# Kernel optimization log

Measured on AMD Instinct MI355X. Metric: run time of the kernel, lower is better.

Reference implementation:

```python
import jax, jax.numpy as jnp
import numpy as np
from jax import lax

# Module config (matches init_kwargs)
C_IN, C_OUT, D_STATE = 512, 256, 16
D_INNER = 2 * C_OUT          # canonical Mamba expand=2
DT_RANK = C_OUT // 16        # ceil(256/16) = 16
D_CONV = 4
BN_EPS = 1e-5


def setup_inputs() -> dict:
    key = jax.random.key(0)
    ks = jax.random.split(key, 16)
    s = 0.02
    B, H, W = 8, 64, 64
    inp = {
        "x": jax.random.normal(ks[0], (B, C_IN, H, W), jnp.float32),
        # lateral 1x1 conv
        "lateral_w": jax.random.normal(ks[1], (C_OUT, C_IN), jnp.float32) * s,
        "lateral_b": jnp.zeros((C_OUT,), jnp.float32),
        # mamba block params
        "in_proj_w": jax.random.normal(ks[2], (2 * D_INNER, C_OUT), jnp.float32) * s,
        "conv1d_w": jax.random.normal(ks[3], (D_INNER, D_CONV), jnp.float32) * s,
        "conv1d_b": jnp.zeros((D_INNER,), jnp.float32),
        "x_proj_w": jax.random.normal(ks[4], (DT_RANK + 2 * D_STATE, D_INNER), jnp.float32) * s,
        "dt_proj_w": jax.random.normal(ks[5], (D_INNER, DT_RANK), jnp.float32) * s,
        "dt_proj_b": jnp.full((D_INNER,), -4.0, jnp.float32),  # softplus -> small dt
        "A_log": jnp.log(jnp.broadcast_to(jnp.arange(1, D_STATE + 1, dtype=jnp.float32), (D_INNER, D_STATE))),  # S4D-real init
        "D_param": jnp.ones((D_INNER,), jnp.float32),
        "out_proj_w": jax.random.normal(ks[6], (C_OUT, D_INNER), jnp.float32) * s,
        # refine: 3x3 conv + BN (eval) + ReLU
        "refine_w": jax.random.normal(ks[7], (C_OUT, C_OUT, 3, 3), jnp.float32) * s,
        "refine_b": jnp.zeros((C_OUT,), jnp.float32),
        "bn_gamma": jnp.ones((C_OUT,), jnp.float32),
        "bn_beta": jnp.zeros((C_OUT,), jnp.float32),
        "bn_mean": jnp.zeros((C_OUT,), jnp.float32),
        "bn_var": jnp.ones((C_OUT,), jnp.float32),
    }
    return inp


def _silu(v):
    return v * jax.nn.sigmoid(v)


def _mamba(u, in_proj_w, conv1d_w, conv1d_b, x_proj_w, dt_proj_w, dt_proj_b,
           A_log, D_param, out_proj_w):
    """Canonical Mamba block on u: (B, L, D) -> (B, L, D)."""
    B, L, D = u.shape
    xz = jnp.einsum('bld,ed->ble', u, in_proj_w)            # (B,L,2*d_inner)
    xm, z = jnp.split(xz, 2, axis=-1)
    # causal depthwise conv1d over L
    xc = xm.transpose(0, 2, 1)                               # (B,d_inner,L)
    xc = lax.conv_general_dilated(xc, conv1d_w[:, None, :], (1,),
                                  [(D_CONV - 1, 0)],
                                  feature_group_count=D_INNER)
    xc = _silu(xc + conv1d_b[None, :, None]).transpose(0, 2, 1)  # (B,L,d_inner)
    proj = jnp.einsum('bld,ed->ble', xc, x_proj_w)           # (B,L,dt_rank+2*N)
    dt_r = proj[..., :DT_RANK]
    B_ssm = proj[..., DT_RANK:DT_RANK + D_STATE]             # (B,L,N)
    C_ssm = proj[..., DT_RANK + D_STATE:]                    # (B,L,N)
    dt = jax.nn.softplus(jnp.einsum('blr,dr->bld', dt_r, dt_proj_w) + dt_proj_b)
    A = -jnp.exp(A_log)                                      # (d_inner,N)

    def step(h, inputs):
        dt_t, B_t, C_t, x_t = inputs                         # (B,d), (B,N), (B,N), (B,d)
        dA = jnp.exp(dt_t[..., None] * A)                    # (B,d,N)
        h = dA * h + dt_t[..., None] * B_t[:, None, :] * x_t[..., None]
        y = jnp.einsum('bdn,bn->bd', h, C_t)
        return h, y

    xs = (dt.transpose(1, 0, 2), B_ssm.transpose(1, 0, 2),
          C_ssm.transpose(1, 0, 2), xc.transpose(1, 0, 2))
    h0 = jnp.zeros((B, D_INNER, D_STATE), u.dtype)
    _, ys = lax.scan(step, h0, xs)                           # (L,B,d_inner)
    y = ys.transpose(1, 0, 2) + xc * D_param
    y = y * _silu(z)
    return jnp.einsum('ble,de->bld', y, out_proj_w)          # (B,L,D)


def reference(x, lateral_w, lateral_b, in_proj_w, conv1d_w, conv1d_b, x_proj_w,
              dt_proj_w, dt_proj_b, A_log, D_param, out_proj_w, refine_w,
              refine_b, bn_gamma, bn_beta, bn_mean, bn_var):
    B, _, H, W = x.shape
    # lateral 1x1 conv
    xl = jnp.einsum('oi,bihw->bohw', lateral_w, x) + lateral_b[None, :, None, None]
    # mamba on flattened spatial sequence, residual add
    u = xl.reshape(B, C_OUT, H * W).transpose(0, 2, 1)        # (B,L,C)
    m = _mamba(u, in_proj_w, conv1d_w, conv1d_b, x_proj_w, dt_proj_w,
               dt_proj_b, A_log, D_param, out_proj_w)
    xr = xl + m.transpose(0, 2, 1).reshape(B, C_OUT, H, W)
    # refine: 3x3 conv + BN(eval) + ReLU
    r = lax.conv_general_dilated(xr, refine_w, (1, 1), [(1, 1), (1, 1)])
    r = r + refine_b[None, :, None, None]
    inv = bn_gamma / jnp.sqrt(bn_var + BN_EPS)
    r = (r - bn_mean[None, :, None, None]) * inv[None, :, None, None] + bn_beta[None, :, None, None]
    return jax.nn.relu(r)
```

## Files before the change

### kernel.cpp

```cpp
#include <hip/hip_runtime.h>
#include <math.h>

#define NB   8
#define CIN  512
#define COUT 256
#define DIN  512
#define LHW  4096
#define NCHK 128
#define CHL  32
#define PW   66
#define PPOS (PW*PW)

typedef __attribute__((ext_vector_type(8))) short bf16x8;
typedef __attribute__((ext_vector_type(4))) float f32x4;
typedef __attribute__((ext_vector_type(2))) float f32x2;

__device__ __forceinline__ float siluf(float v)  { return v / (1.f + __expf(-v)); }
__device__ __forceinline__ float splusf(float v) {
  return fmaxf(v, 0.f) + __logf(1.f + __expf(-fabsf(v)));
}

__device__ __forceinline__ unsigned short f2b(float f) {
  union { float f; unsigned u; } v; v.f = f;
  unsigned r = v.u + 0x7fff + ((v.u >> 16) & 1);
  return (unsigned short)(r >> 16);
}
__device__ __forceinline__ float b2f(unsigned int u) {
  union { unsigned u; float f; } v; v.u = (u & 0xffffu) << 16; return v.f;
}

__device__ __forceinline__ f32x2 pk_fma(f32x2 a, f32x2 b, f32x2 c) {
  f32x2 d;
  asm("v_pk_fma_f32 %0, %1, %2, %3" : "=v"(d) : "v"(a), "v"(b), "v"(c));
  return d;
}
__device__ __forceinline__ f32x2 pk_mul(f32x2 a, f32x2 b) {
  f32x2 d;
  asm("v_pk_mul_f32 %0, %1, %2" : "=v"(d) : "v"(a), "v"(b));
  return d;
}

__device__ __forceinline__ void gload16(const unsigned short* g, unsigned short* l) {
  __builtin_amdgcn_global_load_lds(
      (const __attribute__((address_space(1))) unsigned int*)g,
      (__attribute__((address_space(3))) unsigned int*)l, 16, 0, 0);
}

#define WO1 131072
#define WO2 393216
#define WO3 425984
#define WO4 557056
#define WO5 1146880
__global__ __launch_bounds__(256)
void k_wprep(const float* __restrict__ lw, const float* __restrict__ ipw,
             const float* __restrict__ xpw, const float* __restrict__ opw,
             const float* __restrict__ rw, const float* __restrict__ dtpw,
             unsigned short* __restrict__ wb, unsigned short* __restrict__ wfb) {
  const int i = blockIdx.x * 256 + threadIdx.x;
  if (i < WO1)      wb[i] = f2b(lw[i]);
  else if (i < WO2) wb[i] = f2b(ipw[i - WO1]);
  else if (i < WO3) {
    const int j = i - WO2, row = j >> 9, col = j & 511;
    wb[i] = (row < 48) ? f2b(xpw[row * 512 + col]) : (unsigned short)0;
  }
  else if (i < WO4) wb[i] = f2b(opw[i - WO3]);
  else if (i < WO5) {
    const int j = i - WO4, o = j / 2304, kk = j % 2304;
    const int tap = kk >> 8, ch = kk & 255;
    wb[i] = f2b(rw[(o * 256 + ch) * 9 + tap]);
  }
  else {
    const int j = i - WO5, row = j >> 9, e = j & 511;
    float v = 0.f;
    if (row < 512) {
#pragma unroll
      for (int r = 0; r < 16; ++r)
        v = fmaf(dtpw[row * 16 + r], xpw[r * 512 + e], v);
    } else if (row < 560) {
      v = xpw[(row - 512) * 512 + e];
    }
    wfb[j] = f2b(v);
  }
}

__global__ __launch_bounds__(256)
void k_xpose(const float* __restrict__ x, unsigned short* __restrict__ xt) {
  __shared__ unsigned short Ts[64][80];
  const int b  = blockIdx.z;
  const int k0 = blockIdx.y * 64;
  const int l0 = blockIdx.x * 64;
  const int t  = threadIdx.x;
  const int tx = t & 15, ty = t >> 4;
#pragma unroll
  for (int r = 0; r < 4; ++r) {
    const int k = ty + r * 16;
    float4 v = *(const float4*)(x + ((size_t)b * CIN + k0 + k) * LHW + l0 + tx * 4);
    Ts[tx*4+0][k] = f2b(v.x);
    Ts[tx*4+1][k] = f2b(v.y);
    Ts[tx*4+2][k] = f2b(v.z);
    Ts[tx*4+3][k] = f2b(v.w);
  }
  __syncthreads();
  const int lr = t >> 2, kc = (t & 3) * 16;
  unsigned short* dst = xt + ((size_t)b * LHW + l0 + lr) * CIN + k0 + kc;
  *(uint4*)dst       = *(const uint4*)&Ts[lr][kc];
  *(uint4*)(dst + 8) = *(const uint4*)&Ts[lr][kc + 8];
}

template<int RSA, int RSB, int KTOT>
__device__ __forceinline__ void gemm_loop_128(
    const unsigned short* __restrict__ Ab, const unsigned short* __restrict__ Bb,
    unsigned short (&As)[2][4096], unsigned short (&Bs)[2][4096],
    int t, f32x4 acc[4][4]) {
  const int w = t >> 6, lane = t & 63;
  const int wm = w >> 1, wn = w & 1;
  const int arow = t >> 2;
  const int acol = (((t & 3) ^ ((t >> 3) & 3))) * 8;
  const int fr = lane & 15;
  const int g8 = ((lane >> 4) * 8) ^ (((fr >> 1) & 3) * 8);
  for (int k0 = 0; k0 < KTOT; k0 += 64) {
    __syncthreads();
    gload16(Ab + (size_t)arow * RSA + k0 + acol,             &As[0][w * 512]);
    gload16(Ab + (size_t)(64 + arow) * RSA + k0 + acol,      &As[0][2048 + w*512]);
    gload16(Bb + (size_t)arow * RSB + k0 + acol,             &Bs[0][w * 512]);
    gload16(Bb + (size_t)(64 + arow) * RSB + k0 + acol,      &Bs[0][2048 + w*512]);
    gload16(Ab + (size_t)arow * RSA + k0 + 32 + acol,        &As[1][w * 512]);
    gload16(Ab + (size_t)(64 + arow) * RSA + k0 + 32 + acol, &As[1][2048 + w*512]);
    gload16(Bb + (size_t)arow * RSB + k0 + 32 + acol,        &Bs[1][w * 512]);
    gload16(Bb + (size_t)(64 + arow) * RSB + k0 + 32 + acol, &Bs[1][2048 + w*512]);
    __syncthreads();
#pragma unroll
    for (int h = 0; h < 2; ++h) {
      bf16x8 af[4], bf[4];
#pragma unroll
      for (int f = 0; f < 4; ++f) {
        af[f] = *(const bf16x8*)&As[h][(wm*64 + f*16 + fr) * 32 + g8];
        bf[f] = *(const bf16x8*)&Bs[h][(wn*64 + f*16 + fr) * 32 + g8];
      }
#pragma unroll
      for (int i = 0; i < 4; ++i)
#pragma unroll
        for (int j = 0; j < 4; ++j)
          acc[i][j] = __builtin_amdgcn_mfma_f32_16x16x32_bf16(af[i], bf[j], acc[i][j], 0, 0, 0);
    }
  }
}

__global__ __launch_bounds__(256)
void k_lat_mfma(const unsigned short* __restrict__ xt, const unsigned short* __restrict__ lwb,
                const float* __restrict__ lb, unsigned short* __restrict__ ub) {
  __shared__ __align__(16) unsigned short As[2][4096], Bs[2][4096];
  const int t = threadIdx.x, lane = t & 63, w = t >> 6;
  const int wm = w >> 1, wn = w & 1;
  const int b = blockIdx.z, m0 = blockIdx.y * 128, n0 = blockIdx.x * 128;
  f32x4 acc[4][4] = {};
  gemm_loop_128<512, 512, 512>(xt + ((size_t)b * LHW + m0) * 512,
                               lwb + (size_t)n0 * 512, As, Bs, t, acc);
  const int fr = lane & 15, q4 = (lane >> 4) * 4;
#pragma unroll
  for (int i = 0; i < 4; ++i) {
    const int l = m0 + wm*64 + i*16 + q4;
#pragma unroll
    for (int j = 0; j < 4; ++j) {
      const int o = n0 + wn*64 + j*16 + fr;
      const float bias = lb[o];
      unsigned short* dst = ub + ((size_t)b * LHW + l) * COUT + o;
#pragma unroll
      for (int q = 0; q < 4; ++q)
        dst[(size_t)q * COUT] = f2b(acc[i][j][q] + bias);
    }
  }
}

__global__ __launch_bounds__(256)
void k_inproj_mfma(const unsigned short* __restrict__ ub, const unsigned short* __restrict__ ipwb,
                   unsigned short* __restrict__ xm_b, unsigned short* __restrict__ zsb) {
  __shared__ __align__(16) unsigned short As[2][4096], Bs[2][4096];
  const int t = threadIdx.x, lane = t & 63, w = t >> 6;
  const int wm = w >> 1, wn = w & 1;
  const int b = blockIdx.z, m0 = blockIdx.y * 128, n0 = blockIdx.x * 128;
  f32x4 acc[4][4] = {};
  gemm_loop_128<256, 256, 256>(ub + ((size_t)b * LHW + m0) * 256,
                               ipwb + (size_t)n0 * 256, As, Bs, t, acc);
  const int fr = lane & 15, q4 = (lane >> 4) * 4;
  const bool isz = (n0 >= 512);
#pragma unroll
  for (int i = 0; i < 4; ++i) {
    const int l = m0 + wm*64 + i*16 + q4;
#pragma unroll
    for (int j = 0; j < 4; ++j) {
      const int e = n0 + wn*64 + j*16 + fr;
      if (isz) {
        unsigned short* dst = zsb + ((size_t)b * LHW + l) * DIN + (e - 512);
#pragma unroll
        for (int q = 0; q < 4; ++q)
          dst[(size_t)q * DIN] = f2b(siluf(acc[i][j][q]));
      } else {
        unsigned short* dst = xm_b + ((size_t)b * LHW + l) * DIN + e;
#pragma unroll
        for (int q = 0; q < 4; ++q)
          dst[(size_t)q * DIN] = f2b(acc[i][j][q]);
      }
    }
  }
}

__global__ __launch_bounds__(256)
void k_conv1d(const unsigned short* __restrict__ xm_b, const float* __restrict__ cw,
              const float* __restrict__ cb, unsigned short* __restrict__ xc_b) {
  const int tid = blockIdx.x * 256 + threadIdx.x;
  const int e8 = tid & 63;
  const int lg = tid >> 6;
  const int l0 = (lg & 511) * 8;
  const int b  = lg >> 9;
  const int e0 = e8 * 8;
  float bias[8];
  *(float4*)&bias[0] = *(const float4*)(cb + e0);
  *(float4*)&bias[4] = *(const float4*)(cb + e0 + 4);
  float wv[8][4];
#pragma unroll
  for (int q = 0; q < 8; ++q) {
    float4 w4 = *(const float4*)(cw + (e0 + q) * 4);
    wv[q][0] = w4.x; wv[q][1] = w4.y; wv[q][2] = w4.z; wv[q][3] = w4.w;
  }
  const unsigned short* base = xm_b + ((size_t)b * LHW + l0) * DIN + e0;
  uint4 rows[11];
  const uint4 z4 = make_uint4(0u, 0u, 0u, 0u);
#pragma unroll
  for (int r = 0; r < 11; ++r) {
    const int ll = r - 3;
    rows[r] = (l0 + ll >= 0) ? *(const uint4*)(base + (ptrdiff_t)ll * DIN) : z4;
  }
  unsigned short* outb = xc_b + ((size_t)b * LHW + l0) * DIN + e0;
#pragma unroll
  for (int j = 0; j < 8; ++j) {
    float acc[8];
#pragma unroll
    for (int q = 0; q < 8; ++q) acc[q] = bias[q];
#pragma unroll
    for (int k = 0; k < 4; ++k) {
      const uint4 raw = rows[j + k];
      acc[0] = fmaf(b2f(raw.x),       wv[0][k], acc[0]);
      acc[1] = fmaf(b2f(raw.x >> 16), wv[1][k], acc[1]);
      acc[2] = fmaf(b2f(raw.y),       wv[2][k], acc[2]);
      acc[3] = fmaf(b2f(raw.y >> 16), wv[3][k], acc[3]);
      acc[4] = fmaf(b2f(raw.z),       wv[4][k], acc[4]);
      acc[5] = fmaf(b2f(raw.z >> 16), wv[5][k], acc[5]);
      acc[6] = fmaf(b2f(raw.w),       wv[6][k], acc[6]);
      acc[7] = fmaf(b2f(raw.w >> 16), wv[7][k], acc[7]);
    }
    uint4 o;
    o.x = (unsigned)f2b(siluf(acc[0])) | ((unsigned)f2b(siluf(acc[1])) << 16);
    o.y = (unsigned)f2b(siluf(acc[2])) | ((unsigned)f2b(siluf(acc[3])) << 16);
    o.z = (unsigned)f2b(siluf(acc[4])) | ((unsigned)f2b(siluf(acc[5])) << 16);
    o.w = (unsigned)f2b(siluf(acc[6])) | ((unsigned)f2b(siluf(acc[7])) << 16);
    *(uint4*)(outb + (size_t)j * DIN) = o;
  }
}

__global__ __launch_bounds__(256)
void k_xdt_mfma(const unsigned short* __restrict__ xc_b, const unsigned short* __restrict__ wfb,
                const float* __restrict__ dtpb,
                unsigned short* __restrict__ dtb, float* __restrict__ proj) {
  __shared__ __align__(16) unsigned short As[2][4096], Bs[2][4096];
  const int t = threadIdx.x, lane = t & 63, w = t >> 6;
  const int wm = w >> 1, wn = w & 1;
  const int b = blockIdx.z, m0 = blockIdx.x * 128, n0 = blockIdx.y * 128;
  f32x4 acc[4][4] = {};
  gemm_loop_128<512, 512, 512>(xc_b + ((size_t)b * LHW + m0) * 512,
                               wfb + (size_t)n0 * 512, As, Bs, t, acc);
  const int fr = lane & 15, q4 = (lane >> 4) * 4;
#pragma unroll
  for (int i = 0; i < 4; ++i) {
    const int l = m0 + wm*64 + i*16 + q4;
#pragma unroll
    for (int j = 0; j < 4; ++j) {
      const int c = n0 + wn*64 + j*16 + fr;
      if (c < 512) {
        const float bias = dtpb[c];
        unsigned short* dst = dtb + ((size_t)b * LHW + l) * 512 + c;
#pragma unroll
        for (int q = 0; q < 4; ++q)
          dst[(size_t)q * 512] = f2b(splusf(acc[i][j][q] + bias));
      } else if (c < 560) {
        float* dst = proj + ((size_t)b * LHW + l) * 48 + (c - 512);
#pragma unroll
        for (int q = 0; q < 4; ++q)
          dst[(size_t)q * 48] = acc[i][j][q];
      }
    }
  }
}

__global__ __launch_bounds__(512, 4)
void k_scanA(const float* __restrict__ proj, const unsigned short* __restrict__ dtb,
             const unsigned short* __restrict__ xc_b, const float* __restrict__ A_log,
             float* __restrict__ Sst, float* __restrict__ SDT) {
  __shared__ float prs[CHL * 16];
  const int bx = blockIdx.x;
  const int b = bx >> 7, c = bx & 127;
  const int d = threadIdx.x;
  const size_t rbase = (size_t)b * LHW + c * CHL;
  for (int i = d; i < CHL * 4; i += 512) {
    const int row = i >> 2, c4 = i & 3;
    *(float4*)&prs[row * 16 + c4 * 4] = *(const float4*)(proj + (rbase + row) * 48 + 16 + c4 * 4);
  }
  float An[16];
#pragma unroll
  for (int q = 0; q < 4; ++q) {
    float4 a4 = *(const float4*)(A_log + d*16 + q*4);
    An[q*4+0] = -__expf(a4.x); An[q*4+1] = -__expf(a4.y);
    An[q*4+2] = -__expf(a4.z); An[q*4+3] = -__expf(a4.w);
  }
  f32x2 h2[8];
#pragma unroll
  for (int k = 0; k < 8; ++k) h2[k] = (f32x2){0.f, 0.f};
  const float An0 = An[0];
  bool lin = true;
#pragma unroll
  for (int n = 1; n < 16; ++n)
    lin = lin && (fabsf(An[n] - (n + 1) * An0) <= 1e-4f * fabsf(An[n]));
  float sdt = 0.f;
  const unsigned short* dt0 = dtb + rbase * 512 + d;
  const unsigned short* xc0 = xc_b + rbase * DIN + d;
  __syncthreads();
  for (int i = 0; i < CHL; ++i) {
    const float dt = b2f(dt0[(size_t)i * 512]);
    sdt += dt;
    const float dtx = dt * b2f(xc0[(size_t)i * DIN]);
    const f32x2 dtx2 = (f32x2){dtx, dtx};
    f32x2 dA2[8];
    if (lin) {
      const float e1 = __expf(dt * An0);
      const float e2 = e1*e1, e3 = e2*e1, e4 = e2*e2, e8 = e4*e4;
      const f32x2 e4v = (f32x2){e4, e4}, e8v = (f32x2){e8, e8};
      dA2[0] = (f32x2){e1, e2};
      dA2[1] = (f32x2){e3, e4};
      dA2[2] = pk_mul(dA2[0], e4v);
      dA2[3] = pk_mul(dA2[1], e4v);
      dA2[4] = pk_mul(dA2[0], e8v);
      dA2[5] = pk_mul(dA2[1], e8v);
      dA2[6] = pk_mul(dA2[2], e8v);
      dA2[7] = pk_mul(dA2[3], e8v);
    } else {
#pragma unroll
      for (int k = 0; k < 8; ++k)
        dA2[k] = (f32x2){__expf(dt * An[2*k]), __expf(dt * An[2*k+1])};
    }
    const f32x2* B2 = (const f32x2*)&prs[i * 16];
#pragma unroll
    for (int k = 0; k < 8; ++k)
      h2[k] = pk_fma(dA2[k], h2[k], pk_mul(dtx2, B2[k]));
  }
  float* o = Sst + ((size_t)bx * 512 + d) * 16;
#pragma unroll
  for (int k = 0; k < 4; ++k)
    *(float4*)(o + k*4) = make_float4(h2[2*k].x, h2[2*k].y, h2[2*k+1].x, h2[2*k+1].y);
  SDT[(size_t)bx * 512 + d] = sdt;
}

__global__ __launch_bounds__(256)
void k_scanB(const float* __restrict__ Sst, const float* __restrict__ SDT,
             const float* __restrict__ A_log, float* __restrict__ hst) {
  const int tid = blockIdx.x * 256 + threadIdx.x;
  const int n = tid & 15;
  const int d = (tid >> 4) & 511;
  const int b = tid >> 13;
  const float An = -__expf(A_log[d * 16 + n]);
  float h = 0.f;
  for (int c = 0; c < NCHK; ++c) {
    const size_t idx = (size_t)((b*NCHK + c)*512 + d);
    hst[idx*16 + n] = h;
    h = __expf(SDT[idx] * An) * h + Sst[idx*16 + n];
  }
}

__global__ __launch_bounds__(512, 4)
void k_scanC(const float* __restrict__ proj, const unsigned short* __restrict__ dtb,
             const unsigned short* __restrict__ xc_b,
             const unsigned short* __restrict__ zsb, const float* __restrict__ hst,
             const float* __restrict__ A_log, const float* __restrict__ Dpar,
             unsigned short* __restrict__ ydata) {
  __shared__ float prs[CHL * 32];
  const int bx = blockIdx.x;
  const int b = bx >> 7, c = bx & 127;
  const int d = threadIdx.x;
  const size_t rbase = (size_t)b * LHW + c * CHL;
  for (int i = d; i < CHL * 8; i += 512) {
    const int row = i >> 3, c4 = i & 7;
    *(float4*)&prs[row * 32 + c4 * 4] = *(const float4*)(proj + (rbase + row) * 48 + 16 + c4 * 4);
  }
  float An[16];
#pragma unroll
  for (int q = 0; q < 4; ++q) {
    float4 a4 = *(const float4*)(A_log + d*16 + q*4);
    An[q*4+0] = -__expf(a4.x); An[q*4+1] = -__expf(a4.y);
    An[q*4+2] = -__expf(a4.z); An[q*4+3] = -__expf(a4.w);
  }
  f32x2 h2[8];
  {
    const float* hsrc = hst + ((size_t)bx * 512 + d) * 16;
#pragma unroll
    for (int k = 0; k < 8; ++k)
      h2[k] = *(const f32x2*)(hsrc + 2*k);
  }
  const float An0 = An[0];
  bool lin = true;
#pragma unroll
  for (int n = 1; n < 16; ++n)
    lin = lin && (fabsf(An[n] - (n + 1) * An0) <= 1e-4f * fabsf(An[n]));
  const float dp = Dpar[d];
  const unsigned short* dt0 = dtb + rbase * 512 + d;
  const unsigned short* xc0 = xc_b + rbase * DIN + d;
  const unsigned short* zs0 = zsb + rbase * DIN + d;
  unsigned short* y0 = ydata + rbase * DIN + d;
  __syncthreads();
  for (int i = 0; i < CHL; ++i) {
    const float dt = b2f(dt0[(size_t)i * 512]);
    const float xt = b2f(xc0[(size_t)i * DIN]);
    const float zv = b2f(zs0[(size_t)i * DIN]);
    const float dtx = dt * xt;
    const f32x2 dtx2 = (f32x2){dtx, dtx};
    f32x2 dA2[8];
    if (lin) {
      const float e1 = __expf(dt * An0);
      const float e2 = e1*e1, e3 = e2*e1, e4 = e2*e2, e8 = e4*e4;
      const f32x2 e4v = (f32x2){e4, e4}, e8v = (f32x2){e8, e8};
      dA2[0] = (f32x2){e1, e2};
      dA2[1] = (f32x2){e3, e4};
      dA2[2] = pk_mul(dA2[0], e4v);
      dA2[3] = pk_mul(dA2[1], e4v);
      dA2[4] = pk_mul(dA2[0], e8v);
      dA2[5] = pk_mul(dA2[1], e8v);
      dA2[6] = pk_mul(dA2[2], e8v);
      dA2[7] = pk_mul(dA2[3], e8v);
    } else {
#pragma unroll
      for (int k = 0; k < 8; ++k)
        dA2[k] = (f32x2){__expf(dt * An[2*k]), __expf(dt * An[2*k+1])};
    }
    const f32x2* B2 = (const f32x2*)&prs[i * 32];
    const f32x2* C2 = (const f32x2*)&prs[i * 32 + 16];
    f32x2 ya = (f32x2){0.f, 0.f}, yb = (f32x2){0.f, 0.f};
#pragma unroll
    for (int k = 0; k < 8; ++k) {
      h2[k] = pk_fma(dA2[k], h2[k], pk_mul(dtx2, B2[k]));
      if (k & 1) yb = pk_fma(h2[k], C2[k], yb);
      else       ya = pk_fma(h2[k], C2[k], ya);
    }
    const float y = (ya.x + ya.y) + (yb.x + yb.y);
    const float ov = (y + xt * dp) * zv;
    y0[(size_t)i * DIN] = f2b(ov);
  }
}

__global__ __launch_bounds__(256)
void k_outproj_mfma(const unsigned short* __restrict__ ydata, const unsigned short* __restrict__ opwb,
                    const unsigned short* __restrict__ ub, unsigned short* __restrict__ xrp) {
  __shared__ __align__(16) unsigned short As[2][4096], Bs[2][4096];
  const int t = threadIdx.x, lane = t & 63, w = t >> 6;
  const int wm = w >> 1, wn = w & 1;
  const int b = blockIdx.z, m0 = blockIdx.y * 128, n0 = blockIdx.x * 128;
  f32x4 acc[4][4] = {};
  gemm_loop_128<512, 512, 512>(ydata + ((size_t)b * LHW + m0) * 512,
                               opwb + (size_t)n0 * 512, As, Bs, t, acc);
  const int fr = lane & 15, q4 = (lane >> 4) * 4;
#pragma unroll
  for (int i = 0; i < 4; ++i) {
    const int lbase = m0 + wm*64 + i*16 + q4;
#pragma unroll
    for (int q = 0; q < 4; ++q) {
      const int l = lbase + q;
      const int pos = ((l >> 6) + 1) * PW + (l & 63) + 1;
#pragma unroll
      for (int j = 0; j < 4; ++j) {
        const int o = n0 + wn*64 + j*16 + fr;
        const float r = b2f(ub[((size_t)b * LHW + l) * COUT + o]);
        xrp[((size_t)b * PPOS + pos) * COUT + o] = f2b(acc[i][j][q] + r);
      }
    }
  }
}

__global__ __launch_bounds__(256)
void k_refine_mfma(const unsigned short* __restrict__ Aw,
                   const unsigned short* __restrict__ xrp,
                   const float* __restrict__ rb, const float* __restrict__ bng,
                   const float* __restrict__ bnb, const float* __restrict__ bnm,
                   const float* __restrict__ bnv, float* __restrict__ out) {
  __shared__ __align__(16) unsigned short As[4][4096], Bs[4][4096];
  const int t = threadIdx.x;
  const int lane = t & 63;
  const int w = t >> 6;
  const int wm = w >> 1, wn = w & 1;
  const int b  = blockIdx.z;
  const int m0 = blockIdx.y * 128;
  const int n0 = blockIdx.x * 128;
  const int y0 = n0 >> 6;
  const unsigned short* xb = xrp + (size_t)b * PPOS * COUT;
  const int arow = t >> 2;
  const int acol = (((t & 3) ^ ((t >> 3) & 3))) * 8;
  const int fr = lane & 15;
  const int g8 = ((lane >> 4) * 8) ^ (((fr >> 1) & 3) * 8);

#define RF_STAGE(ks, buf) {                                                            \
    const int tap_ = (ks) >> 3;                                                        \
    const int i0_  = ((ks) & 7) * 32;                                                  \
    const int ky_  = tap_ / 3, kx_ = tap_ - ky_ * 3;                                   \
    const int k0_  = tap_ * 256 + i0_;                                                 \
    const unsigned short* ga_ = Aw + (size_t)(m0 + arow) * 2304 + k0_ + acol;          \
    const unsigned short* gb_ = xb + ((size_t)((y0 + ky_) * PW + kx_ + arow)) * COUT + i0_ + acol; \
    gload16(ga_,              &As[buf][w * 512]);                                      \
    gload16(ga_ + 64 * 2304,  &As[buf][2048 + w * 512]);                               \
    gload16(gb_,              &Bs[buf][w * 512]);                                      \
    gload16(gb_ + PW * COUT,  &Bs[buf][2048 + w * 512]);                               \
  }

  f32x4 acc[4][4] = {};
  for (int ks = 0; ks < 72; ks += 4) {
    __syncthreads();
    RF_STAGE(ks, 0);
    RF_STAGE(ks + 1, 1);
    RF_STAGE(ks + 2, 2);
    RF_STAGE(ks + 3, 3);
    __syncthreads();
#pragma unroll
    for (int h = 0; h < 4; ++h) {
      bf16x8 af[4], bfr[4];
#pragma unroll
      for (int f = 0; f < 4; ++f) {
        af[f]  = *(const bf16x8*)&As[h][(wm*64 + f*16 + fr) * 32 + g8];
        bfr[f] = *(const bf16x8*)&Bs[h][(wn*64 + f*16 + fr) * 32 + g8];
      }
#pragma unroll
      for (int i = 0; i < 4; ++i)
#pragma unroll
        for (int j = 0; j < 4; ++j)
          acc[i][j] = __builtin_amdgcn_mfma_f32_16x16x32_bf16(af[i], bfr[j], acc[i][j], 0, 0, 0);
    }
  }
#undef RF_STAGE
  const int q4 = (lane >> 4) * 4;
#pragma unroll
  for (int i = 0; i < 4; ++i) {
    const int obase = m0 + wm*64 + i*16 + q4;
#pragma unroll
    for (int q = 0; q < 4; ++q) {
      const int o = obase + q;
      const float inv = bng[o] * rsqrtf(bnv[o] + 1e-5f);
      const float sh  = (rb[o] - bnm[o]) * inv + bnb[o];
      float* orow = out + ((size_t)b * COUT + o) * LHW + n0 + wn*64 + fr;
#pragma unroll
      for (int j = 0; j < 4; ++j)
        orow[j*16] = fmaxf(fmaf(acc[i][j][q], inv, sh), 0.f);
    }
  }
}

extern "C" void kernel_launch(void* const* d_in, const int* in_sizes, int n_in,
                              void* d_out, int out_size, void* d_ws, size_t ws_size,
                              hipStream_t stream) {
  const float* x    = (const float*)d_in[0];
  const float* lw   = (const float*)d_in[1];
  const float* lb   = (const float*)d_in[2];
  const float* ipw  = (const float*)d_in[3];
  const float* cw   = (const float*)d_in[4];
  const float* cb   = (const float*)d_in[5];
  const float* xpw  = (const float*)d_in[6];
  const float* dtpw = (const float*)d_in[7];
  const float* dtpb = (const float*)d_in[8];
  const float* Alog = (const float*)d_in[9];
  const float* Dpar = (const float*)d_in[10];
  const float* opw  = (const float*)d_in[11];
  const float* rw   = (const float*)d_in[12];
  const float* rb   = (const float*)d_in[13];
  const float* bng  = (const float*)d_in[14];
  const float* bnb  = (const float*)d_in[15];
  const float* bnm  = (const float*)d_in[16];
  const float* bnv  = (const float*)d_in[17];
  float* out = (float*)d_out;

  float* ws = (float*)d_ws;
  unsigned short* ub   = (unsigned short*)ws;
  unsigned short* xt   = (unsigned short*)(ws + 4194304);
  unsigned short* xm_b = (unsigned short*)(ws + 12582912);
  unsigned short* xc_b = (unsigned short*)(ws + 20971520);
  unsigned short* zsb  = (unsigned short*)(ws + 29360128);
  float* proj = ws + 37748736;
  float* Sst  = ws + 39321600;
  float* SDT  = ws + 47710208;
  float* hst  = ws + 48234496;
  unsigned short* wb  = (unsigned short*)(ws + 64487424);
  unsigned short* wfb = (unsigned short*)(ws + 65060864);
  unsigned short* lwb  = wb;
  unsigned short* ipwb = wb + WO1;
  unsigned short* opwb = wb + WO3;
  unsigned short* Aw   = wb + WO4;
  unsigned short* ydata = xm_b;
  unsigned short* dtb   = xt;
  unsigned short* xrp   = xt;

  k_wprep<<<dim3(5760), 256, 0, stream>>>(lw, ipw, xpw, opw, rw, dtpw, wb, wfb);
  k_xpose<<<dim3(64, 8, 8), 256, 0, stream>>>(x, xt);
  k_lat_mfma<<<dim3(2, 32, 8), 256, 0, stream>>>(xt, lwb, lb, ub);
  k_inproj_mfma<<<dim3(8, 32, 8), 256, 0, stream>>>(ub, ipwb, xm_b, zsb);
  k_conv1d<<<dim3(1024), 256, 0, stream>>>(xm_b, cw, cb, xc_b);
  k_xdt_mfma<<<dim3(32, 5, 8), 256, 0, stream>>>(xc_b, wfb, dtpb, dtb, proj);
  k_scanA<<<dim3(NB * NCHK), 512, 0, stream>>>(proj, dtb, xc_b, Alog, Sst, SDT);
  k_scanB<<<dim3(256), 256, 0, stream>>>(Sst, SDT, Alog, hst);
  k_scanC<<<dim3(NB * NCHK), 512, 0, stream>>>(proj, dtb, xc_b, zsb, hst, Alog, Dpar, ydata);
  hipMemsetAsync(xrp, 0, (size_t)NB * PPOS * COUT * sizeof(unsigned short), stream);
  k_outproj_mfma<<<dim3(2, 32, 8), 256, 0, stream>>>(ydata, opwb, ub, xrp);
  k_refine_mfma<<<dim3(32, 2, 8), 256, 0, stream>>>(Aw, xrp, rb, bng, bnb, bnm, bnv, out);
}
```

Measured before the change: 343.4 us.

## Halve scan chunk length and store inter-chunk states in bf16

Doubles the number of scan chunks (CHL 32 to 16), so the chunked scan kernels get twice as many blocks with half the serial length each. The chunk-final and carried-in states are stored as bf16 instead of fp32, which offsets the doubled state traffic. The cost is a longer serial inter-chunk pass in scanB (256 steps instead of 128), more state reads and writes overall, and bf16 rounding of the recurrent state, which can hurt accuracy.

```diff
diff --git a/kernel.cpp b/kernel.cpp
--- a/kernel.cpp
+++ b/kernel.cpp
@@ -6,8 +6,8 @@
 #define COUT 256
 #define DIN  512
 #define LHW  4096
-#define NCHK 128
-#define CHL  32
+#define NCHK 256
+#define CHL  16
 #define PW   66
 #define PPOS (PW*PW)
 
@@ -295,10 +295,10 @@
 __global__ __launch_bounds__(512, 4)
 void k_scanA(const float* __restrict__ proj, const unsigned short* __restrict__ dtb,
              const unsigned short* __restrict__ xc_b, const float* __restrict__ A_log,
-             float* __restrict__ Sst, float* __restrict__ SDT) {
+             unsigned short* __restrict__ Sst, float* __restrict__ SDT) {
   __shared__ float prs[CHL * 16];
   const int bx = blockIdx.x;
-  const int b = bx >> 7, c = bx & 127;
+  const int b = bx >> 8, c = bx & 255;
   const int d = threadIdx.x;
   const size_t rbase = (size_t)b * LHW + c * CHL;
   for (int i = d; i < CHL * 4; i += 512) {
@@ -352,16 +352,24 @@
     for (int k = 0; k < 8; ++k)
       h2[k] = pk_fma(dA2[k], h2[k], pk_mul(dtx2, B2[k]));
   }
-  float* o = Sst + ((size_t)bx * 512 + d) * 16;
-#pragma unroll
-  for (int k = 0; k < 4; ++k)
-    *(float4*)(o + k*4) = make_float4(h2[2*k].x, h2[2*k].y, h2[2*k+1].x, h2[2*k+1].y);
+  unsigned short* o = Sst + ((size_t)bx * 512 + d) * 16;
+  uint4 p0, p1;
+  p0.x = (unsigned)f2b(h2[0].x) | ((unsigned)f2b(h2[0].y) << 16);
+  p0.y = (unsigned)f2b(h2[1].x) | ((unsigned)f2b(h2[1].y) << 16);
+  p0.z = (unsigned)f2b(h2[2].x) | ((unsigned)f2b(h2[2].y) << 16);
+  p0.w = (unsigned)f2b(h2[3].x) | ((unsigned)f2b(h2[3].y) << 16);
+  p1.x = (unsigned)f2b(h2[4].x) | ((unsigned)f2b(h2[4].y) << 16);
+  p1.y = (unsigned)f2b(h2[5].x) | ((unsigned)f2b(h2[5].y) << 16);
+  p1.z = (unsigned)f2b(h2[6].x) | ((unsigned)f2b(h2[6].y) << 16);
+  p1.w = (unsigned)f2b(h2[7].x) | ((unsigned)f2b(h2[7].y) << 16);
+  *(uint4*)o       = p0;
+  *(uint4*)(o + 8) = p1;
   SDT[(size_t)bx * 512 + d] = sdt;
 }
 
 __global__ __launch_bounds__(256)
-void k_scanB(const float* __restrict__ Sst, const float* __restrict__ SDT,
-             const float* __restrict__ A_log, float* __restrict__ hst) {
+void k_scanB(const unsigned short* __restrict__ Sst, const float* __restrict__ SDT,
+             const float* __restrict__ A_log, unsigned short* __restrict__ hst) {
   const int tid = blockIdx.x * 256 + threadIdx.x;
   const int n = tid & 15;
   const int d = (tid >> 4) & 511;
@@ -370,20 +378,20 @@
   float h = 0.f;
   for (int c = 0; c < NCHK; ++c) {
     const size_t idx = (size_t)((b*NCHK + c)*512 + d);
-    hst[idx*16 + n] = h;
-    h = __expf(SDT[idx] * An) * h + Sst[idx*16 + n];
+    hst[idx*16 + n] = f2b(h);
+    h = __expf(SDT[idx] * An) * h + b2f(Sst[idx*16 + n]);
   }
 }
 
 __global__ __launch_bounds__(512, 4)
 void k_scanC(const float* __restrict__ proj, const unsigned short* __restrict__ dtb,
              const unsigned short* __restrict__ xc_b,
-             const unsigned short* __restrict__ zsb, const float* __restrict__ hst,
+             const unsigned short* __restrict__ zsb, const unsigned short* __restrict__ hst,
              const float* __restrict__ A_log, const float* __restrict__ Dpar,
              unsigned short* __restrict__ ydata) {
   __shared__ float prs[CHL * 32];
   const int bx = blockIdx.x;
-  const int b = bx >> 7, c = bx & 127;
+  const int b = bx >> 8, c = bx & 255;
   const int d = threadIdx.x;
   const size_t rbase = (size_t)b * LHW + c * CHL;
   for (int i = d; i < CHL * 8; i += 512) {
@@ -399,10 +407,17 @@
   }
   f32x2 h2[8];
   {
-    const float* hsrc = hst + ((size_t)bx * 512 + d) * 16;
-#pragma unroll
-    for (int k = 0; k < 8; ++k)
-      h2[k] = *(const f32x2*)(hsrc + 2*k);
+    const unsigned short* hsrc = hst + ((size_t)bx * 512 + d) * 16;
+    uint4 p0 = *(const uint4*)hsrc;
+    uint4 p1 = *(const uint4*)(hsrc + 8);
+    h2[0] = (f32x2){b2f(p0.x), b2f(p0.x >> 16)};
+    h2[1] = (f32x2){b2f(p0.y), b2f(p0.y >> 16)};
+    h2[2] = (f32x2){b2f(p0.z), b2f(p0.z >> 16)};
+    h2[3] = (f32x2){b2f(p0.w), b2f(p0.w >> 16)};
+    h2[4] = (f32x2){b2f(p1.x), b2f(p1.x >> 16)};
+    h2[5] = (f32x2){b2f(p1.y), b2f(p1.y >> 16)};
+    h2[6] = (f32x2){b2f(p1.z), b2f(p1.z >> 16)};
+    h2[7] = (f32x2){b2f(p1.w), b2f(p1.w >> 16)};
   }
   const float An0 = An[0];
   bool lin = true;
@@ -587,9 +602,9 @@
   unsigned short* xc_b = (unsigned short*)(ws + 20971520);
   unsigned short* zsb  = (unsigned short*)(ws + 29360128);
   float* proj = ws + 37748736;
-  float* Sst  = ws + 39321600;
+  unsigned short* Sst = (unsigned short*)(ws + 39321600);
   float* SDT  = ws + 47710208;
-  float* hst  = ws + 48234496;
+  unsigned short* hst = (unsigned short*)(ws + 48758784);
   unsigned short* wb  = (unsigned short*)(ws + 64487424);
   unsigned short* wfb = (unsigned short*)(ws + 65060864);
   unsigned short* lwb  = wb;
```

New measurement: 336.4 us. 2.0% less time.
